# Performance work log

Measured on AMD Instinct MI355X. Metric: run time of the kernel, lower is better.

The kernel has to match this reference:

```python
import jax, jax.numpy as jnp
import numpy as np

B = 1      # layer math only broadcasts for batch_size == 1
E = 384    # encoding_len = prod(input_shape[1:])


def setup_inputs() -> dict:
    key = jax.random.key(0)
    k1, k2, k3 = jax.random.split(key, 3)
    x = jax.random.normal(k1, (B, E), dtype=jnp.float32)
    kernel = jax.random.normal(k2, (B, E, E * E), dtype=jnp.float32) * 0.02
    bias = jax.random.normal(k3, (E, E * E), dtype=jnp.float32) * 0.02
    space = jnp.zeros((B, E, E * E), dtype=jnp.float32)  # persistent state, init zeros
    return {"x": x, "kernel": kernel, "bias": bias, "space": space}


def reference(x, kernel, bias, space):
    Bv, Ev = x.shape
    I = jnp.eye(Ev, dtype=x.dtype)
    inv_sqrt2 = jnp.asarray(1.0 / np.sqrt(2.0), dtype=x.dtype)
    # kron(x_flat (1,E), I (E,E)) -> (E, E*E): kron[k, j*E+l] = x[0,j] * I[k,l]
    # batched form: [b,k,j,l] = x[b,j] * I[k,l], then flatten (j,l) -> E*E columns
    kron = jnp.einsum('bj,kl->bkjl', x, I).reshape(Bv, Ev, Ev * Ev) * inv_sqrt2
    updated_space = space + kernel * kron + bias[None, :, :]
    # einsum 'bQW,bQ->bQW': scale each row Q of the memory by the input entry
    target = updated_space * x[:, :, None]
    # softmax over axis=1 (rows E), then max over the E*E columns
    out = jnp.max(jax.nn.softmax(target, axis=1), axis=-1)
    return out.reshape(Bv, Ev)
```

## Files before the change

### kernel.cpp

```cpp
#include <hip/hip_runtime.h>
#include <hip/hip_bf16.h>
#include <math.h>


#define E    384
#define CW   (E * E)
#define CB   16
#define NWG  (CW / CB)
#define RPT  6
#define WB   36
#define KB   6

__device__ __forceinline__ unsigned enc_f32(float v) {
    unsigned u = __float_as_uint(v);
    return (u & 0x80000000u) ? ~u : (u | 0x80000000u);
}
__device__ __forceinline__ float dec_f32(unsigned e) {
    unsigned u = (e & 0x80000000u) ? (e ^ 0x80000000u) : ~e;
    return __uint_as_float(u);
}

__global__ __launch_bounds__(256, 6) void gm_main(
    const float* __restrict__ x, const float* __restrict__ kern,
    const float* __restrict__ bias, const float* __restrict__ space,
    float* __restrict__ pw, unsigned* __restrict__ aws, int use_atomic)
{
    __shared__ float ps[4][CB];
    __shared__ float Lc[CB];

    const int t   = threadIdx.x;
    const int wg  = blockIdx.x;
    const int c0  = wg * CB;
    const int j   = c0 / E;
    const int ls  = c0 % E;
    const int g   = t & 3;
    const int rb  = t >> 2;
    const int cbase = c0 + 4 * g;
    const float xj = x[j] * 0.70710678118654752440f;

    float val[RPT][4];
    float s0 = 0.f, s1 = 0.f, s2 = 0.f, s3 = 0.f;

    #pragma unroll
    for (int ch = 0; ch < 2; ++ch) {
        float4 b4[3], p4[3];
        float  xr[3];
        #pragma unroll
        for (int q = 0; q < 3; ++q) {
            const int r    = rb + 64 * (3 * ch + q);
            const int base = r * CW + cbase;
            b4[q] = *(const float4*)(bias  + base);
            p4[q] = *(const float4*)(space + base);
            xr[q] = x[r];
        }
        #pragma unroll
        for (int q = 0; q < 3; ++q) {
            const int qq = 3 * ch + q;
            const int r  = rb + 64 * qq;
            float v0 = b4[q].x + p4[q].x;
            float v1 = b4[q].y + p4[q].y;
            float v2 = b4[q].z + p4[q].z;
            float v3 = b4[q].w + p4[q].w;
            const int cl = r - ls - 4 * g;
            if (cl >= 0 && cl < 4) {
                const float kd = kern[r * CW + cbase + cl] * xj;
                if      (cl == 0) v0 += kd;
                else if (cl == 1) v1 += kd;
                else if (cl == 2) v2 += kd;
                else              v3 += kd;
            }
            v0 *= xr[q]; v1 *= xr[q]; v2 *= xr[q]; v3 *= xr[q];
            val[qq][0] = v0; val[qq][1] = v1;
            val[qq][2] = v2; val[qq][3] = v3;
            s0 += __expf(v0); s1 += __expf(v1);
            s2 += __expf(v2); s3 += __expf(v3);
        }
    }

    #pragma unroll
    for (int m = 4; m <= 32; m <<= 1) {
        s0 += __shfl_xor(s0, m, 64);
        s1 += __shfl_xor(s1, m, 64);
        s2 += __shfl_xor(s2, m, 64);
        s3 += __shfl_xor(s3, m, 64);
    }
    const int wave = t >> 6;
    if ((t & 63) < 4) {
        ps[wave][4 * g + 0] = s0;
        ps[wave][4 * g + 1] = s1;
        ps[wave][4 * g + 2] = s2;
        ps[wave][4 * g + 3] = s3;
    }
    __syncthreads();
    if (t < CB)
        Lc[t] = __logf(ps[0][t] + ps[1][t] + ps[2][t] + ps[3][t]);
    __syncthreads();

    const float l0 = Lc[4 * g + 0], l1 = Lc[4 * g + 1];
    const float l2 = Lc[4 * g + 2], l3 = Lc[4 * g + 3];
    #pragma unroll
    for (int qq = 0; qq < RPT; ++qq) {
        float rm = fmaxf(fmaxf(val[qq][0] - l0, val[qq][1] - l1),
                         fmaxf(val[qq][2] - l2, val[qq][3] - l3));
        rm = fmaxf(rm, __shfl_xor(rm, 1, 64));
        rm = fmaxf(rm, __shfl_xor(rm, 2, 64));
        if (g == 0) {
            const int r = rb + 64 * qq;
            if (use_atomic) atomicMax(aws + r, enc_f32(rm));
            else            pw[wg * E + r] = rm;
        }
    }
}

__global__ __launch_bounds__(256) void gm_reduce1(
    const float* __restrict__ pw, float* __restrict__ pw2)
{
    __shared__ float sm[256];
    const int t  = threadIdx.x;
    const int kb = blockIdx.x % KB;
    const int wb = blockIdx.x / KB;
    const int k  = kb * 64 + (t & 63);
    const int wl = t >> 6;
    float mx = -INFINITY;
    for (int w = wb * 256 + wl; w < wb * 256 + 256; w += 4)
        mx = fmaxf(mx, pw[w * E + k]);
    sm[t] = mx;
    __syncthreads();
    if (t < 64) {
        mx = fmaxf(fmaxf(sm[t], sm[t + 64]), fmaxf(sm[t + 128], sm[t + 192]));
        pw2[wb * E + kb * 64 + t] = mx;
    }
}

__global__ __launch_bounds__(384) void gm_reduce2(
    const float* __restrict__ pw2, float* __restrict__ out)
{
    const int k = threadIdx.x;
    float mx = -INFINITY;
    #pragma unroll
    for (int wb = 0; wb < WB; ++wb)
        mx = fmaxf(mx, pw2[wb * E + k]);
    out[k] = expf(mx);
}

__global__ __launch_bounds__(384) void gm_final_atomic(
    const unsigned* __restrict__ aws, float* __restrict__ out)
{
    const int k = threadIdx.x;
    out[k] = expf(dec_f32(aws[k]));
}

extern "C" void kernel_launch(void* const* d_in, const int* in_sizes, int n_in,
                              void* d_out, int out_size, void* d_ws, size_t ws_size,
                              hipStream_t stream)
{
    const float* x     = (const float*)d_in[0];
    const float* kern  = (const float*)d_in[1];
    const float* bias  = (const float*)d_in[2];
    const float* space = (const float*)d_in[3];
    float* out = (float*)d_out;

    const size_t pw_elems = (size_t)NWG * E;
    const size_t need = (pw_elems + (size_t)WB * E) * sizeof(float);

    if (ws_size >= need) {
        float* pw  = (float*)d_ws;
        float* pw2 = pw + pw_elems;
        gm_main<<<NWG, 256, 0, stream>>>(x, kern, bias, space, pw, nullptr, 0);
        gm_reduce1<<<KB * WB, 256, 0, stream>>>(pw, pw2);
        gm_reduce2<<<1, 384, 0, stream>>>(pw2, out);
    } else {
        unsigned* aws = (unsigned*)d_ws;
        hipMemsetAsync(aws, 0, E * sizeof(unsigned), stream);
        gm_main<<<NWG, 256, 0, stream>>>(x, kern, bias, space, nullptr, aws, 1);
        gm_final_atomic<<<1, 384, 0, stream>>>(aws, out);
    }
}
```

Measured before the change: 589.9 us.

## Split softmax-max into two passes with fp16 exp intermediate buffer

Replaces the single fused kernel, where each workgroup spans all 384 rows for 16 columns, with a two-pass scheme. Pass 1 computes exp values and stores them as fp16 while writing partial column sums. A small kernel then inverts the summed column totals, and pass 2 rereads the fp16 exps, scales them and takes row maxima. The aim is wider, coalesced row-block tiles instead of tall narrow columns. The cost is an extra write and read of a large fp16 intermediate plus fp16 rounding of the softmax values, and the new path only runs if the workspace is large enough.

```diff
diff --git a/kernel.cpp b/kernel.cpp
--- a/kernel.cpp
+++ b/kernel.cpp
@@ -1,15 +1,26 @@
 #include <hip/hip_runtime.h>
 #include <hip/hip_bf16.h>
+#include <hip/hip_fp16.h>
 #include <math.h>
 
 
 #define E    384
 #define CW   (E * E)
-#define CB   16
-#define NWG  (CW / CB)
-#define RPT  6
-#define WB   36
-#define KB   6
+
+#define RB1  32
+#define CC1  1024
+#define NKB1 (E / RB1)
+#define NCB1 (CW / CC1)
+#define RB2  32
+#define CC2  2048
+#define NKB2 (E / RB2)
+#define NCB2 (CW / CC2)
+
+#define CBF  16
+#define NWGF (CW / CBF)
+#define RPTF 6
+#define WBF  36
+#define KBF  6
 
 __device__ __forceinline__ unsigned enc_f32(float v) {
     unsigned u = __float_as_uint(v);
@@ -20,17 +31,152 @@
     return __uint_as_float(u);
 }
 
-__global__ __launch_bounds__(256, 6) void gm_main(
+__global__ __launch_bounds__(256) void gm_pass1(
+    const float* __restrict__ x, const float* __restrict__ kern,
+    const float* __restrict__ bias, const float* __restrict__ space,
+    float2* __restrict__ e4,
+    float* __restrict__ Sp)
+{
+    const int t  = threadIdx.x;
+    const int cb = blockIdx.x % NCB1;
+    const int kb = blockIdx.x / NCB1;
+    const int c  = cb * CC1 + 4 * t;
+    const int m  = c % E;
+    const int j  = c / E;
+    const float xj = x[j] * 0.70710678118654752440f;
+    const int k0 = kb * RB1;
+
+    float s0 = 0.f, s1 = 0.f, s2 = 0.f, s3 = 0.f;
+
+    for (int rr = 0; rr < RB1; rr += 4) {
+        float4 b4[4], p4[4];
+        #pragma unroll
+        for (int u = 0; u < 4; ++u) {
+            const int k   = k0 + rr + u;
+            const int off = k * CW + c;
+            b4[u] = *(const float4*)(bias  + off);
+            p4[u] = *(const float4*)(space + off);
+        }
+        #pragma unroll
+        for (int u = 0; u < 4; ++u) {
+            const int k = k0 + rr + u;
+            float v0 = b4[u].x + p4[u].x;
+            float v1 = b4[u].y + p4[u].y;
+            float v2 = b4[u].z + p4[u].z;
+            float v3 = b4[u].w + p4[u].w;
+            const int dl = k - m;
+            if ((unsigned)dl < 4u) {
+                const float kd = kern[k * CW + c + dl] * xj;
+                if      (dl == 0) v0 += kd;
+                else if (dl == 1) v1 += kd;
+                else if (dl == 2) v2 += kd;
+                else              v3 += kd;
+            }
+            const float xk = x[k];
+            v0 *= xk; v1 *= xk; v2 *= xk; v3 *= xk;
+            const float e0 = __expf(v0), e1 = __expf(v1);
+            const float e2 = __expf(v2), e3 = __expf(v3);
+            s0 += e0; s1 += e1; s2 += e2; s3 += e3;
+            union { __half2 h[2]; float2 f; } pk;
+            pk.h[0] = __floats2half2_rn(e0, e1);
+            pk.h[1] = __floats2half2_rn(e2, e3);
+            e4[(k * CW + c) >> 2] = pk.f;
+        }
+    }
+    *(float4*)(Sp + kb * CW + c) = make_float4(s0, s1, s2, s3);
+}
+
+__global__ __launch_bounds__(256) void gm_inv(
+    const float* __restrict__ Sp, float* __restrict__ R)
+{
+    const int c = 4 * (blockIdx.x * 256 + threadIdx.x);
+    float4 a = *(const float4*)(Sp + c);
+    #pragma unroll
+    for (int kb = 1; kb < NKB1; ++kb) {
+        const float4 b = *(const float4*)(Sp + kb * CW + c);
+        a.x += b.x; a.y += b.y; a.z += b.z; a.w += b.w;
+    }
+    *(float4*)(R + c) = make_float4(1.f / a.x, 1.f / a.y, 1.f / a.z, 1.f / a.w);
+}
+
+__global__ __launch_bounds__(256) void gm_pass2(
+    const float4* __restrict__ e8,
+    const float* __restrict__ R,
+    float* __restrict__ pw)
+{
+    __shared__ float pm[4][RB2];
+    const int t  = threadIdx.x;
+    const int cb = blockIdx.x % NCB2;
+    const int kb = blockIdx.x / NCB2;
+    const int c  = cb * CC2 + 8 * t;
+    const int k0 = kb * RB2;
+    const int wave = t >> 6;
+    const int lane = t & 63;
+    const float4 ra = *(const float4*)(R + c);
+    const float4 rb = *(const float4*)(R + c + 4);
+
+    for (int rr = 0; rr < RB2; rr += 4) {
+        float4 ev[4];
+        #pragma unroll
+        for (int u = 0; u < 4; ++u) {
+            const int k = k0 + rr + u;
+            ev[u] = e8[(k * CW + c) >> 3];
+        }
+        float mx[4];
+        #pragma unroll
+        for (int u = 0; u < 4; ++u) {
+            const __half2* h = (const __half2*)&ev[u];
+            const float2 f0 = __half22float2(h[0]);
+            const float2 f1 = __half22float2(h[1]);
+            const float2 f2 = __half22float2(h[2]);
+            const float2 f3 = __half22float2(h[3]);
+            const float a0 = fmaxf(f0.x * ra.x, f0.y * ra.y);
+            const float a1 = fmaxf(f1.x * ra.z, f1.y * ra.w);
+            const float a2 = fmaxf(f2.x * rb.x, f2.y * rb.y);
+            const float a3 = fmaxf(f3.x * rb.z, f3.y * rb.w);
+            mx[u] = fmaxf(fmaxf(a0, a1), fmaxf(a2, a3));
+        }
+        #pragma unroll
+        for (int st = 1; st < 64; st <<= 1) {
+            mx[0] = fmaxf(mx[0], __shfl_xor(mx[0], st, 64));
+            mx[1] = fmaxf(mx[1], __shfl_xor(mx[1], st, 64));
+            mx[2] = fmaxf(mx[2], __shfl_xor(mx[2], st, 64));
+            mx[3] = fmaxf(mx[3], __shfl_xor(mx[3], st, 64));
+        }
+        if (lane == 0) {
+            pm[wave][rr + 0] = mx[0]; pm[wave][rr + 1] = mx[1];
+            pm[wave][rr + 2] = mx[2]; pm[wave][rr + 3] = mx[3];
+        }
+    }
+    __syncthreads();
+    if (t < RB2) {
+        const float v = fmaxf(fmaxf(pm[0][t], pm[1][t]),
+                              fmaxf(pm[2][t], pm[3][t]));
+        pw[cb * E + k0 + t] = v;
+    }
+}
+
+__global__ __launch_bounds__(384) void gm_out(
+    const float* __restrict__ pw, float* __restrict__ out)
+{
+    const int k = threadIdx.x;
+    float mx = -INFINITY;
+    #pragma unroll
+    for (int cb = 0; cb < NCB2; ++cb)
+        mx = fmaxf(mx, pw[cb * E + k]);
+    out[k] = mx;
+}
+
+__global__ __launch_bounds__(256, 6) void gm_main_fb(
     const float* __restrict__ x, const float* __restrict__ kern,
     const float* __restrict__ bias, const float* __restrict__ space,
     float* __restrict__ pw, unsigned* __restrict__ aws, int use_atomic)
 {
-    __shared__ float ps[4][CB];
-    __shared__ float Lc[CB];
-
+    __shared__ float ps[4][CBF];
+    __shared__ float Lc[CBF];
     const int t   = threadIdx.x;
     const int wg  = blockIdx.x;
-    const int c0  = wg * CB;
+    const int c0  = wg * CBF;
     const int j   = c0 / E;
     const int ls  = c0 % E;
     const int g   = t & 3;
@@ -38,68 +184,46 @@
     const int cbase = c0 + 4 * g;
     const float xj = x[j] * 0.70710678118654752440f;
 
-    float val[RPT][4];
+    float val[RPTF][4];
     float s0 = 0.f, s1 = 0.f, s2 = 0.f, s3 = 0.f;
-
-    #pragma unroll
-    for (int ch = 0; ch < 2; ++ch) {
-        float4 b4[3], p4[3];
-        float  xr[3];
-        #pragma unroll
-        for (int q = 0; q < 3; ++q) {
-            const int r    = rb + 64 * (3 * ch + q);
-            const int base = r * CW + cbase;
-            b4[q] = *(const float4*)(bias  + base);
-            p4[q] = *(const float4*)(space + base);
-            xr[q] = x[r];
-        }
-        #pragma unroll
-        for (int q = 0; q < 3; ++q) {
-            const int qq = 3 * ch + q;
-            const int r  = rb + 64 * qq;
-            float v0 = b4[q].x + p4[q].x;
-            float v1 = b4[q].y + p4[q].y;
-            float v2 = b4[q].z + p4[q].z;
-            float v3 = b4[q].w + p4[q].w;
-            const int cl = r - ls - 4 * g;
-            if (cl >= 0 && cl < 4) {
-                const float kd = kern[r * CW + cbase + cl] * xj;
-                if      (cl == 0) v0 += kd;
-                else if (cl == 1) v1 += kd;
-                else if (cl == 2) v2 += kd;
-                else              v3 += kd;
-            }
-            v0 *= xr[q]; v1 *= xr[q]; v2 *= xr[q]; v3 *= xr[q];
-            val[qq][0] = v0; val[qq][1] = v1;
-            val[qq][2] = v2; val[qq][3] = v3;
-            s0 += __expf(v0); s1 += __expf(v1);
-            s2 += __expf(v2); s3 += __expf(v3);
-        }
-    }
-
-    #pragma unroll
-    for (int m = 4; m <= 32; m <<= 1) {
-        s0 += __shfl_xor(s0, m, 64);
-        s1 += __shfl_xor(s1, m, 64);
-        s2 += __shfl_xor(s2, m, 64);
-        s3 += __shfl_xor(s3, m, 64);
+    #pragma unroll
+    for (int qq = 0; qq < RPTF; ++qq) {
+        const int r    = rb + 64 * qq;
+        const int base = r * CW + cbase;
+        const float4 b4 = *(const float4*)(bias  + base);
+        const float4 p4 = *(const float4*)(space + base);
+        float v0 = b4.x + p4.x, v1 = b4.y + p4.y;
+        float v2 = b4.z + p4.z, v3 = b4.w + p4.w;
+        const int cl = r - ls - 4 * g;
+        if (cl >= 0 && cl < 4) {
+            const float kd = kern[r * CW + cbase + cl] * xj;
+            if      (cl == 0) v0 += kd;
+            else if (cl == 1) v1 += kd;
+            else if (cl == 2) v2 += kd;
+            else              v3 += kd;
+        }
+        const float xr = x[r];
+        v0 *= xr; v1 *= xr; v2 *= xr; v3 *= xr;
+        val[qq][0] = v0; val[qq][1] = v1; val[qq][2] = v2; val[qq][3] = v3;
+        s0 += __expf(v0); s1 += __expf(v1); s2 += __expf(v2); s3 += __expf(v3);
+    }
+    #pragma unroll
+    for (int mk = 4; mk <= 32; mk <<= 1) {
+        s0 += __shfl_xor(s0, mk, 64); s1 += __shfl_xor(s1, mk, 64);
+        s2 += __shfl_xor(s2, mk, 64); s3 += __shfl_xor(s3, mk, 64);
     }
     const int wave = t >> 6;
     if ((t & 63) < 4) {
-        ps[wave][4 * g + 0] = s0;
-        ps[wave][4 * g + 1] = s1;
-        ps[wave][4 * g + 2] = s2;
-        ps[wave][4 * g + 3] = s3;
+        ps[wave][4 * g + 0] = s0; ps[wave][4 * g + 1] = s1;
+        ps[wave][4 * g + 2] = s2; ps[wave][4 * g + 3] = s3;
     }
     __syncthreads();
-    if (t < CB)
-        Lc[t] = __logf(ps[0][t] + ps[1][t] + ps[2][t] + ps[3][t]);
+    if (t < CBF) Lc[t] = __logf(ps[0][t] + ps[1][t] + ps[2][t] + ps[3][t]);
     __syncthreads();
-
     const float l0 = Lc[4 * g + 0], l1 = Lc[4 * g + 1];
     const float l2 = Lc[4 * g + 2], l3 = Lc[4 * g + 3];
     #pragma unroll
-    for (int qq = 0; qq < RPT; ++qq) {
+    for (int qq = 0; qq < RPTF; ++qq) {
         float rm = fmaxf(fmaxf(val[qq][0] - l0, val[qq][1] - l1),
                          fmaxf(val[qq][2] - l2, val[qq][3] - l3));
         rm = fmaxf(rm, __shfl_xor(rm, 1, 64));
@@ -112,13 +236,13 @@
     }
 }
 
-__global__ __launch_bounds__(256) void gm_reduce1(
+__global__ __launch_bounds__(256) void gm_reduce1_fb(
     const float* __restrict__ pw, float* __restrict__ pw2)
 {
     __shared__ float sm[256];
     const int t  = threadIdx.x;
-    const int kb = blockIdx.x % KB;
-    const int wb = blockIdx.x / KB;
+    const int kb = blockIdx.x % KBF;
+    const int wb = blockIdx.x / KBF;
     const int k  = kb * 64 + (t & 63);
     const int wl = t >> 6;
     float mx = -INFINITY;
@@ -132,13 +256,13 @@
     }
 }
 
-__global__ __launch_bounds__(384) void gm_reduce2(
+__global__ __launch_bounds__(384) void gm_reduce2_fb(
     const float* __restrict__ pw2, float* __restrict__ out)
 {
     const int k = threadIdx.x;
     float mx = -INFINITY;
     #pragma unroll
-    for (int wb = 0; wb < WB; ++wb)
+    for (int wb = 0; wb < WBF; ++wb)
         mx = fmaxf(mx, pw2[wb * E + k]);
     out[k] = expf(mx);
 }
@@ -160,19 +284,33 @@
     const float* space = (const float*)d_in[3];
     float* out = (float*)d_out;
 
-    const size_t pw_elems = (size_t)NWG * E;
-    const size_t need = (pw_elems + (size_t)WB * E) * sizeof(float);
-
-    if (ws_size >= need) {
+    const size_t e_bytes  = (size_t)E * CW * 2;
+    const size_t sp_bytes = (size_t)NKB1 * CW * 4;
+    const size_t r_bytes  = (size_t)CW * 4;
+    const size_t pw_bytes = (size_t)NCB2 * E * 4;
+    const size_t need_main = e_bytes + sp_bytes + r_bytes + pw_bytes;
+    const size_t need_fb = ((size_t)NWGF * E + (size_t)WBF * E) * 4;
+
+    if (ws_size >= need_main) {
+        char* w = (char*)d_ws;
+        float2* e4 = (float2*)w;
+        float*  Sp = (float*)(w + e_bytes);
+        float*  R  = (float*)(w + e_bytes + sp_bytes);
+        float*  pw = (float*)(w + e_bytes + sp_bytes + r_bytes);
+        gm_pass1<<<NKB1 * NCB1, 256, 0, stream>>>(x, kern, bias, space, e4, Sp);
+        gm_inv<<<CW / (256 * 4), 256, 0, stream>>>(Sp, R);
+        gm_pass2<<<NKB2 * NCB2, 256, 0, stream>>>((const float4*)e4, R, pw);
+        gm_out<<<1, 384, 0, stream>>>(pw, out);
+    } else if (ws_size >= need_fb) {
         float* pw  = (float*)d_ws;
-        float* pw2 = pw + pw_elems;
-        gm_main<<<NWG, 256, 0, stream>>>(x, kern, bias, space, pw, nullptr, 0);
-        gm_reduce1<<<KB * WB, 256, 0, stream>>>(pw, pw2);
-        gm_reduce2<<<1, 384, 0, stream>>>(pw2, out);
+        float* pw2 = pw + (size_t)NWGF * E;
+        gm_main_fb<<<NWGF, 256, 0, stream>>>(x, kern, bias, space, pw, nullptr, 0);
+        gm_reduce1_fb<<<KBF * WBF, 256, 0, stream>>>(pw, pw2);
+        gm_reduce2_fb<<<1, 384, 0, stream>>>(pw2, out);
     } else {
         unsigned* aws = (unsigned*)d_ws;
         hipMemsetAsync(aws, 0, E * sizeof(unsigned), stream);
-        gm_main<<<NWG, 256, 0, stream>>>(x, kern, bias, space, nullptr, aws, 1);
+        gm_main_fb<<<NWGF, 256, 0, stream>>>(x, kern, bias, space, nullptr, aws, 1);
         gm_final_atomic<<<1, 384, 0, stream>>>(aws, out);
     }
 }
```

Measured after the change: 579.8 us. About the same (-1.7%).
